# Optimization experiments

Measured on AMD Instinct MI355X. Metric: run time of the kernel, lower is better.

The kernel has to match this reference:

```python
import jax, jax.numpy as jnp
import numpy as np

NUM_HEADS = 16
THETA = 10000.0


def apply_rope(x, pos, theta):
    # x: [B, H, S, d], pos: [S] int
    d = x.shape[-1]
    inv_freq = theta ** (-jnp.arange(0, d, 2, dtype=jnp.float32) / d)  # [d/2]
    ang = pos.astype(jnp.float32)[:, None] * inv_freq  # [S, d/2]
    cos, sin = jnp.cos(ang), jnp.sin(ang)
    x1, x2 = x[..., 0::2], x[..., 1::2]
    out_even = x1 * cos - x2 * sin
    out_odd = x1 * sin + x2 * cos
    return jnp.stack([out_even, out_odd], axis=-1).reshape(x.shape)


def setup_inputs() -> dict:
    key = jax.random.key(0)
    ks = jax.random.split(key, 5)
    B, S, D = 4, 2048, 2048
    s = 1.0 / np.sqrt(D)
    return {
        "x": jax.random.normal(ks[0], (B, S, D), dtype=jnp.float32),
        "token_positions": jnp.arange(S, dtype=jnp.int32),
        "wq": jax.random.normal(ks[1], (D, D), dtype=jnp.float32) * s,
        "wk": jax.random.normal(ks[2], (D, D), dtype=jnp.float32) * s,
        "wv": jax.random.normal(ks[3], (D, D), dtype=jnp.float32) * s,
        "wo": jax.random.normal(ks[4], (D, D), dtype=jnp.float32) * s,
    }


def reference(x, token_positions, wq, wk, wv, wo):
    B, S, _ = x.shape
    H = NUM_HEADS
    dh = wq.shape[0] // H

    def proj(w):
        y = jnp.einsum('bsd,ed->bse', x, w)  # Linear: x @ W^T
        return y.reshape(B, S, H, dh).transpose(0, 2, 1, 3)  # [B,H,S,dh]

    Q, K, V = proj(wq), proj(wk), proj(wv)
    Q = apply_rope(Q, token_positions, THETA)
    K = apply_rope(K, token_positions, THETA)

    scores = jnp.einsum('bhqd,bhkd->bhqk', Q, K) / jnp.sqrt(jnp.float32(dh))
    causal = jnp.tril(jnp.ones((S, S), dtype=bool))
    scores = jnp.where(causal, scores, jnp.finfo(scores.dtype).min)
    attn = jax.nn.softmax(scores, axis=-1)
    out = jnp.einsum('bhqk,bhkd->bhqd', attn, V)
    out = out.transpose(0, 2, 1, 3).reshape(B, S, H * dh)
    return jnp.einsum('bsd,ed->bse', out, wo)
```

## Files before the change

### kernel.cpp

```cpp
#include <hip/hip_runtime.h>
#include <math.h>

typedef __bf16 bf16;
typedef bf16 bf16x8 __attribute__((ext_vector_type(8)));
typedef bf16 bf16x4v __attribute__((ext_vector_type(4)));
typedef float f32x4 __attribute__((ext_vector_type(4)));

#define BB 4
#define SS 2048
#define DD 2048
#define HH 16
#define DH 128

__device__ __forceinline__ void gload_lds16(const bf16* g, bf16* l) {
  __builtin_amdgcn_global_load_lds(
      (const __attribute__((address_space(1))) void*)g,
      (__attribute__((address_space(3))) void*)l, 16, 0, 0);
}

__global__ __launch_bounds__(256) void cast_kernel(const float* __restrict__ in,
                                                   bf16* __restrict__ out, int n4) {
  int i = blockIdx.x * blockDim.x + threadIdx.x;
  if (i < n4) {
    const float4 v = ((const float4*)in)[i];
    bf16x4v o = {(bf16)v.x, (bf16)v.y, (bf16)v.z, (bf16)v.w};
    ((bf16x4v*)out)[i] = o;
  }
}

__global__ __launch_bounds__(256) void cast4_kernel(const float* __restrict__ w0,
                                                    const float* __restrict__ w1,
                                                    const float* __restrict__ w2,
                                                    const float* __restrict__ w3,
                                                    bf16* __restrict__ out) {
  const int i = blockIdx.x * blockDim.x + threadIdx.x;
  const int per = (DD * DD) / 4;
  const int sel = i / per, off = i - sel * per;
  const float* src = (sel == 0) ? w0 : (sel == 1) ? w1 : (sel == 2) ? w2 : w3;
  const float4 v = ((const float4*)src)[off];
  bf16x4v o = {(bf16)v.x, (bf16)v.y, (bf16)v.z, (bf16)v.w};
  ((bf16x4v*)(out + (size_t)sel * DD * DD))[off] = o;
}

template <int MODE>
__global__ __launch_bounds__(512, 2) void gemm256(const bf16* __restrict__ A,
                                                  const bf16* __restrict__ Bw,
                                                  bf16* __restrict__ Cb,
                                                  float* __restrict__ Cf,
                                                  const int* __restrict__ pos,
                                                  int M, int N, int K) {
  __shared__ alignas(16) bf16 lA[2][2][256 * 32];
  __shared__ alignas(16) bf16 lB[2][2][256 * 32];

  const int tid = threadIdx.x;
  const int wave = tid >> 6, lane = tid & 63;
  const int quad = lane >> 4, l15 = lane & 15;
  const int wm = wave >> 2, wn = wave & 3;

  const int lin = blockIdx.y * gridDim.x + blockIdx.x;
  const int swz = (lin & 7) * 32 + (lin >> 3);
  const int m0 = (swz >> 3) * 256, n0 = (swz & 7) * 256;

  auto stageH = [&](bf16* dst, const bf16* src, int rbase, int u, int kh) {
#pragma unroll
    for (int j = 0; j < 2; ++j) {
      const int c = j * 512 + wave * 64 + lane;
      const int row = c >> 2, p = c & 2 * 2 - 1;
      const int kc = p ^ (row & 3);
      gload_lds16(src + (size_t)(rbase + row) * K + u * 64 + kh * 32 + kc * 8,
                  dst + (size_t)(j * 512 + wave * 64) * 8);
    }
  };

  auto rdA = [&](int buf, int kh, int mf) -> bf16x8 {
    const int row = wm * 128 + mf * 16 + l15;
    return *(const bf16x8*)(&lA[buf][kh][0] + row * 32 + ((quad ^ (row & 3)) * 8));
  };
  auto rdB = [&](int buf, int kh, int nf) -> bf16x8 {
    const int row = wn * 64 + nf * 16 + l15;
    return *(const bf16x8*)(&lB[buf][kh][0] + row * 32 + ((quad ^ (row & 3)) * 8));
  };

  f32x4 acc[8][4] = {};
  const int NT = K >> 6;

  stageH(&lA[0][0][0], A, m0, 0, 0);
  stageH(&lB[0][0][0], Bw, n0, 0, 0);
  stageH(&lA[0][1][0], A, m0, 0, 1);
  stageH(&lB[0][1][0], Bw, n0, 0, 1);

  bf16x8 af[8], bfr[2];
  for (int t = 0; t < NT; ++t) {
    const int buf = t & 1;
    const bool pre = (t + 1 < NT);

    asm volatile("s_waitcnt vmcnt(4)" ::: "memory");
    __builtin_amdgcn_s_barrier();
    __builtin_amdgcn_sched_barrier(0);
#pragma unroll
    for (int mf = 0; mf < 8; ++mf) af[mf] = rdA(buf, 0, mf);
    bfr[0] = rdB(buf, 0, 0);
    bfr[1] = rdB(buf, 0, 1);
    if (pre) stageH(&lA[buf ^ 1][0][0], A, m0, t + 1, 0);
    asm volatile("s_waitcnt lgkmcnt(0)" ::: "memory");
    __builtin_amdgcn_sched_barrier(0);
    __builtin_amdgcn_s_setprio(1);
#pragma unroll
    for (int mf = 0; mf < 8; ++mf)
#pragma unroll
      for (int nf = 0; nf < 2; ++nf)
        acc[mf][nf] = __builtin_amdgcn_mfma_f32_16x16x32_bf16(af[mf], bfr[nf], acc[mf][nf], 0, 0, 0);
    __builtin_amdgcn_s_setprio(0);
    __builtin_amdgcn_sched_barrier(0);

    bfr[0] = rdB(buf, 0, 2);
    bfr[1] = rdB(buf, 0, 3);
    if (pre) stageH(&lB[buf ^ 1][0][0], Bw, n0, t + 1, 0);
    asm volatile("s_waitcnt lgkmcnt(0)" ::: "memory");
    __builtin_amdgcn_sched_barrier(0);
    __builtin_amdgcn_s_setprio(1);
#pragma unroll
    for (int mf = 0; mf < 8; ++mf)
#pragma unroll
      for (int nf = 0; nf < 2; ++nf)
        acc[mf][nf + 2] = __builtin_amdgcn_mfma_f32_16x16x32_bf16(af[mf], bfr[nf], acc[mf][nf + 2], 0, 0, 0);
    __builtin_amdgcn_s_setprio(0);
    __builtin_amdgcn_sched_barrier(0);

    if (pre) asm volatile("s_waitcnt vmcnt(4)" ::: "memory");
    else     asm volatile("s_waitcnt vmcnt(0)" ::: "memory");
    __builtin_amdgcn_s_barrier();
    __builtin_amdgcn_sched_barrier(0);
#pragma unroll
    for (int mf = 0; mf < 8; ++mf) af[mf] = rdA(buf, 1, mf);
    bfr[0] = rdB(buf, 1, 0);
    bfr[1] = rdB(buf, 1, 1);
    if (pre) stageH(&lA[buf ^ 1][1][0], A, m0, t + 1, 1);
    asm volatile("s_waitcnt lgkmcnt(0)" ::: "memory");
    __builtin_amdgcn_sched_barrier(0);
    __builtin_amdgcn_s_setprio(1);
#pragma unroll
    for (int mf = 0; mf < 8; ++mf)
#pragma unroll
      for (int nf = 0; nf < 2; ++nf)
        acc[mf][nf] = __builtin_amdgcn_mfma_f32_16x16x32_bf16(af[mf], bfr[nf], acc[mf][nf], 0, 0, 0);
    __builtin_amdgcn_s_setprio(0);
    __builtin_amdgcn_sched_barrier(0);

    bfr[0] = rdB(buf, 1, 2);
    bfr[1] = rdB(buf, 1, 3);
    if (pre) stageH(&lB[buf ^ 1][1][0], Bw, n0, t + 1, 1);
    asm volatile("s_waitcnt lgkmcnt(0)" ::: "memory");
    __builtin_amdgcn_sched_barrier(0);
    __builtin_amdgcn_s_setprio(1);
#pragma unroll
    for (int mf = 0; mf < 8; ++mf)
#pragma unroll
      for (int nf = 0; nf < 2; ++nf)
        acc[mf][nf + 2] = __builtin_amdgcn_mfma_f32_16x16x32_bf16(af[mf], bfr[nf], acc[mf][nf + 2], 0, 0, 0);
    __builtin_amdgcn_s_setprio(0);
    __builtin_amdgcn_sched_barrier(0);
  }

  float ps[8][4];
  if (MODE == 0) {
#pragma unroll
    for (int mf = 0; mf < 8; ++mf)
#pragma unroll
      for (int r = 0; r < 4; ++r)
        ps[mf][r] = (float)pos[(m0 + wm * 128 + mf * 16 + quad * 4 + r) & (SS - 1)];
  }

#pragma unroll
  for (int nf = 0; nf < 4; ++nf) {
    const int col = n0 + wn * 64 + nf * 16 + l15;
    float invf = 0.f, sgn = 0.f;
    if (MODE == 0) {
      const int d = col & (DH - 1);
      invf = exp2f((float)(d >> 1) * (-13.28771238f / 64.0f));
      sgn = (d & 1) ? 1.0f : -1.0f;
    }
#pragma unroll
    for (int mf = 0; mf < 8; ++mf) {
#pragma unroll
      for (int r = 0; r < 4; ++r) {
        const int row = m0 + wm * 128 + mf * 16 + quad * 4 + r;
        float v = acc[mf][nf][r];
        if (MODE == 0) {
          const float partner = __shfl_xor(v, 1);
          float sn, cn;
          __sincosf(ps[mf][r] * invf, &sn, &cn);
          v = fmaf(partner, sgn * sn, v * cn);
          const int b = row >> 11, s = row & (SS - 1);
          const int h = col >> 7, d = col & (DH - 1);
          Cb[((((size_t)b * HH + h) * SS + s) << 7) + d] = (bf16)v;
        } else if (MODE == 1) {
          const int b = row >> 11, s = row & (SS - 1);
          const int h = col >> 7, d = col & (DH - 1);
          Cb[(((size_t)b * HH + h) * DH + d) * SS + s] = (bf16)v;
        } else {
          Cf[(size_t)row * N + col] = v;
        }
      }
    }
  }
}

__global__ __launch_bounds__(256, 2) void flash_attn(const bf16* __restrict__ Q,
                                                     const bf16* __restrict__ Kg,
                                                     const bf16* __restrict__ Vt,
                                                     bf16* __restrict__ O) {
  __shared__ alignas(16) bf16 lK[2][64 * 128];
  __shared__ alignas(16) bf16 lP[4][32 * 64];

  const int tid = threadIdx.x;
  const int wave = tid >> 6, lane = tid & 63;
  const int quad = lane >> 4, l15 = lane & 15;
  const int swz = l15 & 7;

  const int lin = blockIdx.y * gridDim.x + blockIdx.x;
  const int bh = ((lin & 7) << 3) | ((lin >> 3) & 7);
  const int q0 = (15 - (lin >> 6)) * 128;

  const bf16* Qh = Q + (size_t)bh * SS * DH;
  const bf16* Kh = Kg + (size_t)bh * SS * DH;
  const bf16* Vh = Vt + (size_t)bh * DH * SS;
  const int nkb = (q0 >> 6) + 2;
  const int qrow0 = q0 + wave * 32;

  bf16x8 qf[2][4];
#pragma unroll
  for (int qt = 0; qt < 2; ++qt)
#pragma unroll
    for (int t = 0; t < 4; ++t)
      qf[qt][t] = *(const bf16x8*)(Qh + (size_t)(qrow0 + qt * 16 + l15) * DH + t * 32 + quad * 8);

  bf16* lPw = &lP[wave][0];
  const float cs = 0.12751649736f;
  const float MSTAT = 20.0f;
  float lsum[2] = {0.f, 0.f};
  f32x4 oacc[2][8] = {};
  int cur = 0;

  auto stage = [&](int b, int kb) {
#pragma unroll
    for (int j = 0; j < 4; ++j) {
      const int c = tid + j * 256;
      const int kr = c >> 4;
      gload_lds16(Kh + (size_t)(kb * 64 + kr) * DH + (((c & 15) ^ (kr & 7)) * 8),
                  &lK[b][0] + (size_t)(wave * 64 + j * 256) * 8);
    }
  };

  auto kv_iter = [&](int kb, bool masked) {
    int ktlim = 3;
    if (masked) {
      ktlim = (qrow0 + 31 - kb * 64) >> 4;
      if (ktlim < 0) return;
      if (ktlim > 3) ktlim = 3;
    }
    const bf16* kcur = &lK[cur][0];

    f32x4 sacc[2][4];
#pragma unroll
    for (int qt = 0; qt < 2; ++qt)
#pragma unroll
      for (int kt = 0; kt < 4; ++kt) sacc[qt][kt] = (f32x4){0.f, 0.f, 0.f, 0.f};
    __builtin_amdgcn_s_setprio(1);
#pragma unroll
    for (int kt = 0; kt < 4; ++kt) {
      if (kt <= ktlim) {
#pragma unroll
        for (int t = 0; t < 4; ++t) {
          const bf16x8 kfrag =
              *(const bf16x8*)(kcur + (kt * 16 + l15) * 128 + (((t * 4 + quad) ^ swz) * 8));
          sacc[0][kt] = __builtin_amdgcn_mfma_f32_16x16x32_bf16(kfrag, qf[0][t], sacc[0][kt], 0, 0, 0);
          sacc[1][kt] = __builtin_amdgcn_mfma_f32_16x16x32_bf16(kfrag, qf[1][t], sacc[1][kt], 0, 0, 0);
        }
      }
    }
    __builtin_amdgcn_s_setprio(0);

#pragma unroll
    for (int kt = 0; kt < 4; ++kt) {
#pragma unroll
      for (int qt = 0; qt < 2; ++qt) {
        bf16x4v pk = {(bf16)0.f, (bf16)0.f, (bf16)0.f, (bf16)0.f};
        if (kt <= ktlim) {
          float ls = 0.f;
#pragma unroll
          for (int r = 0; r < 4; ++r) {
            float e = exp2f(fmaf(sacc[qt][kt][r], cs, -MSTAT));
            if (masked) {
              const int key = kb * 64 + kt * 16 + quad * 4 + r;
              if (key > qrow0 + qt * 16 + l15) e = 0.f;
            }
            ls += e;
            pk[r] = (bf16)e;
          }
          lsum[qt] += ls;
        }
        *(bf16x4v*)(lPw + (qt * 16 + l15) * 64 + (((kt * 2 + (quad >> 1)) ^ swz) * 8) +
                    (quad & 1) * 4) = pk;
      }
    }

    bf16x8 pa[2][2];
#pragma unroll
    for (int qt = 0; qt < 2; ++qt)
#pragma unroll
      for (int kc = 0; kc < 2; ++kc)
        pa[qt][kc] = *(const bf16x8*)(lPw + (qt * 16 + l15) * 64 + (((kc * 4 + quad) ^ swz) * 8));

    __builtin_amdgcn_s_setprio(1);
#pragma unroll
    for (int g = 0; g < 2; ++g) {
      bf16x8 vf[4][2];
#pragma unroll
      for (int d2 = 0; d2 < 4; ++d2)
#pragma unroll
        for (int kc = 0; kc < 2; ++kc)
          vf[d2][kc] = *(const bf16x8*)(Vh + (size_t)((g * 4 + d2) * 16 + l15) * SS + kb * 64 +
                                        kc * 32 + quad * 8);
#pragma unroll
      for (int d2 = 0; d2 < 4; ++d2)
#pragma unroll
        for (int kc = 0; kc < 2; ++kc) {
          oacc[0][g * 4 + d2] =
              __builtin_amdgcn_mfma_f32_16x16x32_bf16(pa[0][kc], vf[d2][kc], oacc[0][g * 4 + d2], 0, 0, 0);
          oacc[1][g * 4 + d2] =
              __builtin_amdgcn_mfma_f32_16x16x32_bf16(pa[1][kc], vf[d2][kc], oacc[1][g * 4 + d2], 0, 0, 0);
        }
    }
    __builtin_amdgcn_s_setprio(0);
  };

  stage(0, 0);
  __syncthreads();

  for (int kb = 0; kb < nkb - 1; ++kb) {
    stage(cur ^ 1, kb + 1);
    kv_iter(kb, kb + 2 >= nkb);
    __syncthreads();
    cur ^= 1;
  }
  kv_iter(nkb - 1, true);

#pragma unroll
  for (int qt = 0; qt < 2; ++qt) {
    lsum[qt] += __shfl_xor(lsum[qt], 16);
    lsum[qt] += __shfl_xor(lsum[qt], 32);
  }

  const int b = bh >> 4, h = bh & 15;
#pragma unroll
  for (int qt = 0; qt < 2; ++qt) {
#pragma unroll
    for (int r = 0; r < 4; ++r) {
      const int qq = quad * 4 + r;
      const float il = 1.0f / __shfl(lsum[qt], qq);
      bf16* orow = O + ((size_t)b * SS + qrow0 + qt * 16 + qq) * DD + h * DH;
#pragma unroll
      for (int db = 0; db < 8; ++db) orow[db * 16 + l15] = (bf16)(oacc[qt][db][r] * il);
    }
  }
}

extern "C" void kernel_launch(void* const* d_in, const int* in_sizes, int n_in,
                              void* d_out, int out_size, void* d_ws, size_t ws_size,
                              hipStream_t stream) {
  (void)in_sizes; (void)n_in; (void)out_size; (void)ws_size;
  const float* x = (const float*)d_in[0];
  const int* pos = (const int*)d_in[1];
  const float* wq = (const float*)d_in[2];
  const float* wk = (const float*)d_in[3];
  const float* wv = (const float*)d_in[4];
  const float* wo = (const float*)d_in[5];
  float* out = (float*)d_out;

  bf16* xb  = (bf16*)d_ws;
  bf16* wqb = xb + (size_t)BB * SS * DD;
  bf16* wkb = wqb + (size_t)DD * DD;
  bf16* wvb = wkb + (size_t)DD * DD;
  bf16* wob = wvb + (size_t)DD * DD;
  bf16* Qb  = wob + (size_t)DD * DD;
  bf16* Kbf = Qb + (size_t)BB * SS * DD;
  bf16* Vtb = Kbf + (size_t)BB * SS * DD;
  bf16* Ob  = Vtb + (size_t)BB * SS * DD;

  const int nx = BB * SS * DD;
  cast_kernel<<<nx / 4 / 256, 256, 0, stream>>>(x, xb, nx / 4);
  cast4_kernel<<<DD * DD / 256, 256, 0, stream>>>(wq, wk, wv, wo, wqb);

  dim3 gg(DD / 256, (BB * SS) / 256);
  gemm256<0><<<gg, 512, 0, stream>>>(xb, wqb, Qb, nullptr, pos, BB * SS, DD, DD);
  gemm256<0><<<gg, 512, 0, stream>>>(xb, wkb, Kbf, nullptr, pos, BB * SS, DD, DD);
  gemm256<1><<<gg, 512, 0, stream>>>(xb, wvb, Vtb, nullptr, nullptr, BB * SS, DD, DD);

  flash_attn<<<dim3(SS / 128, BB * HH), 256, 0, stream>>>(Qb, Kbf, Vtb, Ob);

  gemm256<2><<<gg, 512, 0, stream>>>(Ob, wob, nullptr, out, nullptr, BB * SS, DD, DD);
}
```

Baseline: 622.7 us.

## Fuse QKV projections into one GEMM, merge casts, prefetch V before QK

Merges the two cast kernels into one launch and fuses the Q, K and V projection GEMMs into a single GEMM over the concatenated weight matrix (N=3*DD). The epilogue applies RoPE for Q/K column blocks and writes V transposed, and the tile swizzle is generalized to the larger grid. In flash attention, all V fragments for the block are loaded from global memory at the start of each iteration, before the next K tile is staged, so their latency overlaps the QK^T and softmax work. This cuts launch count and gives the projection more blocks, at the cost of extra registers for the V fragments.

```diff
diff --git a/kernel.cpp b/kernel.cpp
--- a/kernel.cpp
+++ b/kernel.cpp
@@ -18,28 +18,28 @@
       (__attribute__((address_space(3))) void*)l, 16, 0, 0);
 }
 
-__global__ __launch_bounds__(256) void cast_kernel(const float* __restrict__ in,
-                                                   bf16* __restrict__ out, int n4) {
-  int i = blockIdx.x * blockDim.x + threadIdx.x;
-  if (i < n4) {
-    const float4 v = ((const float4*)in)[i];
-    bf16x4v o = {(bf16)v.x, (bf16)v.y, (bf16)v.z, (bf16)v.w};
-    ((bf16x4v*)out)[i] = o;
-  }
-}
-
-__global__ __launch_bounds__(256) void cast4_kernel(const float* __restrict__ w0,
-                                                    const float* __restrict__ w1,
-                                                    const float* __restrict__ w2,
-                                                    const float* __restrict__ w3,
-                                                    bf16* __restrict__ out) {
+__global__ __launch_bounds__(256) void cast_all(const float* __restrict__ x,
+                                                const float* __restrict__ w0,
+                                                const float* __restrict__ w1,
+                                                const float* __restrict__ w2,
+                                                const float* __restrict__ w3,
+                                                bf16* __restrict__ out) {
   const int i = blockIdx.x * blockDim.x + threadIdx.x;
+  const int nxf = (BB * SS * DD) / 4;
   const int per = (DD * DD) / 4;
-  const int sel = i / per, off = i - sel * per;
-  const float* src = (sel == 0) ? w0 : (sel == 1) ? w1 : (sel == 2) ? w2 : w3;
+  const float* src;
+  int off;
+  if (i < nxf) {
+    src = x; off = i;
+  } else {
+    const int j = i - nxf;
+    const int sel = j >> 20;
+    off = j & (per - 1);
+    src = (sel == 0) ? w0 : (sel == 1) ? w1 : (sel == 2) ? w2 : w3;
+  }
   const float4 v = ((const float4*)src)[off];
   bf16x4v o = {(bf16)v.x, (bf16)v.y, (bf16)v.z, (bf16)v.w};
-  ((bf16x4v*)(out + (size_t)sel * DD * DD))[off] = o;
+  ((bf16x4v*)out)[i] = o;
 }
 
 template <int MODE>
@@ -57,15 +57,17 @@
   const int quad = lane >> 4, l15 = lane & 15;
   const int wm = wave >> 2, wn = wave & 3;
 
+  const int nbc = N >> 8;
   const int lin = blockIdx.y * gridDim.x + blockIdx.x;
-  const int swz = (lin & 7) * 32 + (lin >> 3);
-  const int m0 = (swz >> 3) * 256, n0 = (swz & 7) * 256;
+  const int perx = (gridDim.x * gridDim.y) >> 3;
+  const int swz = (lin & 7) * perx + (lin >> 3);
+  const int m0 = (swz / nbc) * 256, n0 = (swz % nbc) * 256;
 
   auto stageH = [&](bf16* dst, const bf16* src, int rbase, int u, int kh) {
 #pragma unroll
     for (int j = 0; j < 2; ++j) {
       const int c = j * 512 + wave * 64 + lane;
-      const int row = c >> 2, p = c & 2 * 2 - 1;
+      const int row = c >> 2, p = c & 3;
       const int kc = p ^ (row & 3);
       gload_lds16(src + (size_t)(rbase + row) * K + u * 64 + kh * 32 + kc * 8,
                   dst + (size_t)(j * 512 + wave * 64) * 8);
@@ -162,8 +164,9 @@
     __builtin_amdgcn_sched_barrier(0);
   }
 
+  const bool rope_blk = (MODE == 3) && (n0 < 2 * DD);
   float ps[8][4];
-  if (MODE == 0) {
+  if (rope_blk) {
 #pragma unroll
     for (int mf = 0; mf < 8; ++mf)
 #pragma unroll
@@ -175,7 +178,7 @@
   for (int nf = 0; nf < 4; ++nf) {
     const int col = n0 + wn * 64 + nf * 16 + l15;
     float invf = 0.f, sgn = 0.f;
-    if (MODE == 0) {
+    if (rope_blk) {
       const int d = col & (DH - 1);
       invf = exp2f((float)(d >> 1) * (-13.28771238f / 64.0f));
       sgn = (d & 1) ? 1.0f : -1.0f;
@@ -186,18 +189,20 @@
       for (int r = 0; r < 4; ++r) {
         const int row = m0 + wm * 128 + mf * 16 + quad * 4 + r;
         float v = acc[mf][nf][r];
-        if (MODE == 0) {
-          const float partner = __shfl_xor(v, 1);
-          float sn, cn;
-          __sincosf(ps[mf][r] * invf, &sn, &cn);
-          v = fmaf(partner, sgn * sn, v * cn);
+        if (MODE == 3) {
           const int b = row >> 11, s = row & (SS - 1);
-          const int h = col >> 7, d = col & (DH - 1);
-          Cb[((((size_t)b * HH + h) * SS + s) << 7) + d] = (bf16)v;
-        } else if (MODE == 1) {
-          const int b = row >> 11, s = row & (SS - 1);
-          const int h = col >> 7, d = col & (DH - 1);
-          Cb[(((size_t)b * HH + h) * DH + d) * SS + s] = (bf16)v;
+          const int cm = col & (DD - 1);
+          const int h = cm >> 7, d = cm & (DH - 1);
+          if (rope_blk) {
+            const float partner = __shfl_xor(v, 1);
+            float sn, cn;
+            __sincosf(ps[mf][r] * invf, &sn, &cn);
+            v = fmaf(partner, sgn * sn, v * cn);
+            const int mat = col >> 11;
+            Cb[(size_t)mat * BB * SS * DD + ((((size_t)b * HH + h) * SS + s) << 7) + d] = (bf16)v;
+          } else {
+            Cb[(size_t)2 * BB * SS * DD + (((size_t)b * HH + h) * DH + d) * SS + s] = (bf16)v;
+          }
         } else {
           Cf[(size_t)row * N + col] = v;
         }
@@ -252,13 +257,24 @@
     }
   };
 
-  auto kv_iter = [&](int kb, bool masked) {
+  auto kv_iter = [&](int kb, bool masked, bool stage_next) {
     int ktlim = 3;
     if (masked) {
       ktlim = (qrow0 + 31 - kb * 64) >> 4;
       if (ktlim < 0) return;
       if (ktlim > 3) ktlim = 3;
     }
+
+    bf16x8 vf[8][2];
+#pragma unroll
+    for (int d8 = 0; d8 < 8; ++d8)
+#pragma unroll
+      for (int kc = 0; kc < 2; ++kc)
+        vf[d8][kc] = *(const bf16x8*)(Vh + (size_t)(d8 * 16 + l15) * SS + kb * 64 +
+                                      kc * 32 + quad * 8);
+
+    if (stage_next) stage(cur ^ 1, kb + 1);
+
     const bf16* kcur = &lK[cur][0];
 
     f32x4 sacc[2][4];
@@ -314,24 +330,12 @@
 
     __builtin_amdgcn_s_setprio(1);
 #pragma unroll
-    for (int g = 0; g < 2; ++g) {
-      bf16x8 vf[4][2];
-#pragma unroll
-      for (int d2 = 0; d2 < 4; ++d2)
-#pragma unroll
-        for (int kc = 0; kc < 2; ++kc)
-          vf[d2][kc] = *(const bf16x8*)(Vh + (size_t)((g * 4 + d2) * 16 + l15) * SS + kb * 64 +
-                                        kc * 32 + quad * 8);
-#pragma unroll
-      for (int d2 = 0; d2 < 4; ++d2)
-#pragma unroll
-        for (int kc = 0; kc < 2; ++kc) {
-          oacc[0][g * 4 + d2] =
-              __builtin_amdgcn_mfma_f32_16x16x32_bf16(pa[0][kc], vf[d2][kc], oacc[0][g * 4 + d2], 0, 0, 0);
-          oacc[1][g * 4 + d2] =
-              __builtin_amdgcn_mfma_f32_16x16x32_bf16(pa[1][kc], vf[d2][kc], oacc[1][g * 4 + d2], 0, 0, 0);
-        }
-    }
+    for (int d8 = 0; d8 < 8; ++d8)
+#pragma unroll
+      for (int kc = 0; kc < 2; ++kc) {
+        oacc[0][d8] = __builtin_amdgcn_mfma_f32_16x16x32_bf16(pa[0][kc], vf[d8][kc], oacc[0][d8], 0, 0, 0);
+        oacc[1][d8] = __builtin_amdgcn_mfma_f32_16x16x32_bf16(pa[1][kc], vf[d8][kc], oacc[1][d8], 0, 0, 0);
+      }
     __builtin_amdgcn_s_setprio(0);
   };
 
@@ -339,12 +343,11 @@
   __syncthreads();
 
   for (int kb = 0; kb < nkb - 1; ++kb) {
-    stage(cur ^ 1, kb + 1);
-    kv_iter(kb, kb + 2 >= nkb);
+    kv_iter(kb, kb + 2 >= nkb, true);
     __syncthreads();
     cur ^= 1;
   }
-  kv_iter(nkb - 1, true);
+  kv_iter(nkb - 1, true, false);
 
 #pragma unroll
   for (int qt = 0; qt < 2; ++qt) {
@@ -380,24 +383,20 @@
 
   bf16* xb  = (bf16*)d_ws;
   bf16* wqb = xb + (size_t)BB * SS * DD;
-  bf16* wkb = wqb + (size_t)DD * DD;
-  bf16* wvb = wkb + (size_t)DD * DD;
-  bf16* wob = wvb + (size_t)DD * DD;
+  bf16* wob = wqb + (size_t)3 * DD * DD;
   bf16* Qb  = wob + (size_t)DD * DD;
   bf16* Kbf = Qb + (size_t)BB * SS * DD;
   bf16* Vtb = Kbf + (size_t)BB * SS * DD;
   bf16* Ob  = Vtb + (size_t)BB * SS * DD;
 
-  const int nx = BB * SS * DD;
-  cast_kernel<<<nx / 4 / 256, 256, 0, stream>>>(x, xb, nx / 4);
-  cast4_kernel<<<DD * DD / 256, 256, 0, stream>>>(wq, wk, wv, wo, wqb);
-
-  dim3 gg(DD / 256, (BB * SS) / 256);
-  gemm256<0><<<gg, 512, 0, stream>>>(xb, wqb, Qb, nullptr, pos, BB * SS, DD, DD);
-  gemm256<0><<<gg, 512, 0, stream>>>(xb, wkb, Kbf, nullptr, pos, BB * SS, DD, DD);
-  gemm256<1><<<gg, 512, 0, stream>>>(xb, wvb, Vtb, nullptr, nullptr, BB * SS, DD, DD);
+  const int ntot4 = (BB * SS * DD + 4 * DD * DD) / 4;
+  cast_all<<<ntot4 / 256, 256, 0, stream>>>(x, wq, wk, wv, wo, xb);
+
+  gemm256<3><<<dim3(3 * DD / 256, (BB * SS) / 256), 512, 0, stream>>>(
+      xb, wqb, Qb, nullptr, pos, BB * SS, 3 * DD, DD);
 
   flash_attn<<<dim3(SS / 128, BB * HH), 256, 0, stream>>>(Qb, Kbf, Vtb, Ob);
 
-  gemm256<2><<<gg, 512, 0, stream>>>(Ob, wob, nullptr, out, nullptr, BB * SS, DD, DD);
+  gemm256<2><<<dim3(DD / 256, (BB * SS) / 256), 512, 0, stream>>>(
+      Ob, wob, nullptr, out, nullptr, BB * SS, DD, DD);
 }
```

Result: no change. 625.2 us (+0.4%).
